# Performance work log

Measured on AMD Instinct MI355X. Metric: run time of the kernel, lower is better.

Reference implementation:

```python
import jax, jax.numpy as jnp
import numpy as np

N_USERS = 100000
N_ITEMS = 100000
N = N_USERS + N_ITEMS
E = 3200000
TXT = 768
GREC = 16
D = 32            # embedding_dim (hardcoded 32 in the torch module)
LAYERS = 3        # len(weight_size)


def setup_inputs() -> dict:
    key = jax.random.key(0)
    ks = jax.random.split(key, 20)
    inp = {}
    inp["edge_row"] = jax.random.randint(ks[0], (E,), 0, N, dtype=jnp.int32)
    inp["edge_col"] = jax.random.randint(ks[1], (E,), 0, N, dtype=jnp.int32)
    # normalized adjacency values (positive, small)
    inp["adj_vals"] = jax.random.uniform(ks[2], (E,), dtype=jnp.float32) * 0.1
    inp["user_name_embs"] = jax.random.normal(ks[3], (N_USERS, TXT), dtype=jnp.float32)
    inp["sent_embs"] = jax.random.normal(ks[4], (N_ITEMS, TXT), dtype=jnp.float32)
    # learned params
    inp["user_emb"] = jax.random.normal(ks[5], (N_USERS, GREC), dtype=jnp.float32) * 0.1
    inp["item_emb"] = jax.random.normal(ks[6], (N_ITEMS, GREC), dtype=jnp.float32) * 0.1
    inp["ue_W1"] = jax.random.normal(ks[7], (TXT, 32), dtype=jnp.float32) * 0.05
    inp["ue_W2"] = jax.random.normal(ks[8], (32, GREC), dtype=jnp.float32) * 0.05
    inp["ie_W1"] = jax.random.normal(ks[9], (TXT, 32), dtype=jnp.float32) * 0.05
    inp["ie_W2"] = jax.random.normal(ks[10], (32, GREC), dtype=jnp.float32) * 0.05
    inp["gc_W"] = jax.random.normal(ks[11], (LAYERS, D, D), dtype=jnp.float32) * 0.1
    inp["gc_b"] = jnp.zeros((LAYERS, D), dtype=jnp.float32)
    inp["bi_W"] = jax.random.normal(ks[12], (LAYERS, D, D), dtype=jnp.float32) * 0.1
    inp["bi_b"] = jnp.zeros((LAYERS, D), dtype=jnp.float32)
    return inp


def _ngcf_forward(edge_row, edge_col, adj_vals, user_name_embs, sent_embs,
                  user_emb, item_emb, ue_W1, ue_W2, ie_W1, ie_W2,
                  gc_W, gc_b, bi_W, bi_b):
    # text encoders (Dropout is identity in eval mode)
    u_created = jax.nn.relu(user_name_embs @ ue_W1) @ ue_W2   # [Nu, 16]
    i_created = jax.nn.relu(sent_embs @ ie_W1) @ ie_W2         # [Ni, 16]
    agg_user = jnp.concatenate([user_emb, u_created], axis=1)  # [Nu, 32]
    agg_item = jnp.concatenate([item_emb, i_created], axis=1)  # [Ni, 32]
    ego = jnp.concatenate([agg_user, agg_item], axis=0)        # [N, 32]

    all_embeddings = [ego]
    for l in range(LAYERS):
        # sparse.mm(adj, ego): gather source rows, scale by edge value, scatter-add
        gathered = adj_vals[:, None] * ego[edge_col]           # [E, 32]
        side = jax.ops.segment_sum(gathered, edge_row, num_segments=N)  # [N, 32]
        sum_emb = jax.nn.leaky_relu(side @ gc_W[l] + gc_b[l])
        bi_emb = jax.nn.leaky_relu((ego * side) @ bi_W[l] + bi_b[l])
        ego = sum_emb + bi_emb                                 # dropout = identity (eval)
        norm = ego / jnp.maximum(
            jnp.linalg.norm(ego, axis=1, keepdims=True), 1e-12)
        all_embeddings.append(norm)
    return jnp.concatenate(all_embeddings, axis=1)             # [N, 32*(LAYERS+1)]


def reference(edge_row, edge_col, adj_vals, user_name_embs, sent_embs,
              user_emb, item_emb, ue_W1, ue_W2, ie_W1, ie_W2,
              gc_W, gc_b, bi_W, bi_b):
    all_e = _ngcf_forward(edge_row, edge_col, adj_vals, user_name_embs, sent_embs,
                          user_emb, item_emb, ue_W1, ue_W2, ie_W1, ie_W2,
                          gc_W, gc_b, bi_W, bi_b)
    u_g = all_e[:N_USERS]
    i_g = all_e[N_USERS:]
    return (u_g, i_g)
```

## Files before the change

kernel.cpp:

```cpp
#include <hip/hip_runtime.h>
#include <cstdint>

#define NU 100000
#define NI 100000
#define NN 200000
#define NE 3200000
#define TXT 768
#define DD 32
#define NRANGE 8
#define ROWS_PER_RANGE (NN / NRANGE)
#define NBJ 313

typedef _Float16 f16x8 __attribute__((ext_vector_type(8)));
typedef _Float16 f16x4 __attribute__((ext_vector_type(4)));
typedef float    f32x4 __attribute__((ext_vector_type(4)));

typedef __attribute__((address_space(1))) const unsigned int guint;
typedef __attribute__((address_space(3))) unsigned int luint;

__device__ __forceinline__ float lrelu(float x) { return x >= 0.f ? x : 0.01f * x; }

__global__ __launch_bounds__(256) void prep_kernel(
    const int* __restrict__ erow,
    const float* __restrict__ uemb, const float* __restrict__ iemb,
    const float* __restrict__ ueW1, const float* __restrict__ ieW1,
    int* __restrict__ cnt,
    _Float16* __restrict__ ego16, float* __restrict__ outp,
    _Float16* __restrict__ w1p)
{
    const int b = blockIdx.x;
    const int tid = threadIdx.x;

    if (b < 2504) {
        const int rlo = (b & 7) * ROWS_PER_RANGE;
        const int rhi = rlo + ROWS_PER_RANGE;
        const int bj  = b >> 3;
        const int4* e4 = (const int4*)erow;
        for (int c = bj * 256 + tid; c < NE / 4; c += NBJ * 256) {
            int4 v = e4[c];
            if (v.x >= rlo && v.x < rhi) atomicAdd(&cnt[v.x], 1);
            if (v.y >= rlo && v.y < rhi) atomicAdd(&cnt[v.y], 1);
            if (v.z >= rlo && v.z < rhi) atomicAdd(&cnt[v.z], 1);
            if (v.w >= rlo && v.w < rhi) atomicAdd(&cnt[v.w], 1);
        }
    } else if (b < 2504 + 3125) {
        int idx = (b - 2504) * 256 + tid;
        if (idx >= NN * 4) return;
        int n = idx >> 2, q = idx & 3;
        float4 v;
        if (n < NU) v = ((const float4*)uemb)[(size_t)n * 4 + q];
        else        v = ((const float4*)iemb)[(size_t)(n - NU) * 4 + q];
        f16x4 h;
        h[0] = (_Float16)v.x; h[1] = (_Float16)v.y;
        h[2] = (_Float16)v.z; h[3] = (_Float16)v.w;
        *(f16x4*)(ego16 + (size_t)n * 32 + q * 4) = h;
        ((float4*)outp)[(size_t)n * 32 + q] = v;
    } else {
        int i = (b - 5629) * 256 + tid;
        int side = (i >= 24576);
        int ii = i - side * 24576;
        const float* W1 = side ? ieW1 : ueW1;
        int j   = ii & 7;
        int ln  = (ii >> 3) & 63;
        int kbH = ii >> 9;
        int kb  = kbH >> 1, H = kbH & 1;
        int k   = kb * 32 + (ln >> 4) * 8 + j;
        int c   = H * 16 + (ln & 15);
        w1p[i] = (_Float16)W1[k * 32 + c];
    }
}

__global__ __launch_bounds__(512, 4) void mlp_mfma_v3(
    const float* __restrict__ Xu, const float* __restrict__ Xi,
    const _Float16* __restrict__ w1pack,
    const float* __restrict__ ueW2, const float* __restrict__ ieW2,
    _Float16* __restrict__ ego16,
    float* __restrict__ outp)
{
    __shared__ float sbuf[16384];

    const int tid  = threadIdx.x;
    const int lane = tid & 63;
    const int wv   = tid >> 6;

    const bool isU = blockIdx.x < 512;
    const float* X  = isU ? Xu : Xi;
    const _Float16* w1p = w1pack + (isU ? 0 : 24576);
    const float* W2 = isU ? ueW2 : ieW2;
    const int node_base = isU ? 0 : NU;
    const int bj = isU ? blockIdx.x : blockIdx.x - 512;

    const int r16 = lane & 15;
    const int cg  = lane >> 4;
    const int rx  = r16 & 7;

    f16x8 bw2;
    #pragma unroll
    for (int j = 0; j < 8; ++j)
        bw2[j] = (_Float16)W2[((lane >> 4) * 8 + j) * 16 + (lane & 15)];

    float* wbuf = &sbuf[wv * 2048];

#define STAGE(bufidx, cc) do {                                                   \
        _Pragma("unroll")                                                        \
        for (int i_ = 0; i_ < 4; ++i_) {                                         \
            int r_ = i_ * 4 + (lane >> 4);                                       \
            int s_ = (lane & 15) ^ (r_ & 7);                                     \
            const float* g_ = xtile + (size_t)r_ * TXT + (cc) * 64 + s_ * 4;     \
            __builtin_amdgcn_global_load_lds((guint*)g_,                         \
                (luint*)(wbuf + (bufidx) * 1024 + i_ * 256), 16, 0, 0);          \
        }                                                                        \
    } while (0)

    const int gw = bj * 8 + wv;
    const int t0 = (int)(((long)gw * 6250) >> 12);
    const int t1 = (int)(((long)(gw + 1) * 6250) >> 12);

    for (int tile = t0; tile < t1; ++tile) {
        const float* xtile = X + (size_t)tile * 16 * TXT;
        asm volatile("s_waitcnt lgkmcnt(0)" ::: "memory");
        STAGE(0, 0);
        STAGE(1, 1);

        f32x4 c0 = {0.f, 0.f, 0.f, 0.f};
        f32x4 c1 = {0.f, 0.f, 0.f, 0.f};

        #pragma unroll
        for (int c = 0; c < 12; ++c) {
            if (c == 11) asm volatile("s_waitcnt vmcnt(0)" ::: "memory");
            else         asm volatile("s_waitcnt vmcnt(4)" ::: "memory");

            #pragma unroll
            for (int k2 = 0; k2 < 2; ++k2) {
                const int kb = c * 2 + k2;
                f16x8 b0 = *(const f16x8*)&w1p[(kb * 2 + 0) * 512 + lane * 8];
                f16x8 b1 = *(const f16x8*)&w1p[(kb * 2 + 1) * 512 + lane * 8];
                const int s0 = k2 * 8 + cg * 2;
                const float* p0 = wbuf + (c & 1) * 1024 + (r16 * 16 + (s0 ^ rx)) * 4;
                const float* p1 = wbuf + (c & 1) * 1024 + (r16 * 16 + ((s0 + 1) ^ rx)) * 4;
                f32x4 xa = *(const f32x4*)p0;
                f32x4 xb = *(const f32x4*)p1;
                f16x8 a;
                a[0] = (_Float16)xa[0]; a[1] = (_Float16)xa[1];
                a[2] = (_Float16)xa[2]; a[3] = (_Float16)xa[3];
                a[4] = (_Float16)xb[0]; a[5] = (_Float16)xb[1];
                a[6] = (_Float16)xb[2]; a[7] = (_Float16)xb[3];
                c0 = __builtin_amdgcn_mfma_f32_16x16x32_f16(a, b0, c0, 0, 0, 0);
                c1 = __builtin_amdgcn_mfma_f32_16x16x32_f16(a, b1, c1, 0, 0, 0);
            }
            if (c < 10) {
                asm volatile("s_waitcnt lgkmcnt(0)" ::: "memory");
                STAGE(c & 1, c + 2);
            }
        }

        _Float16* hb = (_Float16*)wbuf;
        #pragma unroll
        for (int j = 0; j < 4; ++j) {
            int r = (lane >> 4) * 4 + j;
            hb[r * 40 + (lane & 15)]      = (_Float16)fmaxf(c0[j], 0.f);
            hb[r * 40 + (lane & 15) + 16] = (_Float16)fmaxf(c1[j], 0.f);
        }
        const _Float16* ap = &hb[(lane & 15) * 40 + (lane >> 4) * 8];
        f16x4 lo = *(const f16x4*)ap;
        f16x4 hi = *(const f16x4*)(ap + 4);
        f16x8 a2;
        a2[0] = lo[0]; a2[1] = lo[1]; a2[2] = lo[2]; a2[3] = lo[3];
        a2[4] = hi[0]; a2[5] = hi[1]; a2[6] = hi[2]; a2[7] = hi[3];

        f32x4 c2 = {0.f, 0.f, 0.f, 0.f};
        c2 = __builtin_amdgcn_mfma_f32_16x16x32_f16(a2, bw2, c2, 0, 0, 0);

        const int rbase = node_base + tile * 16 + (lane >> 4) * 4;
        const int j2 = lane & 15;
        #pragma unroll
        for (int j = 0; j < 4; ++j) {
            float v = c2[j];
            ego16[(size_t)(rbase + j) * 32  + 16 + j2] = (_Float16)v;
            outp [(size_t)(rbase + j) * 128 + 16 + j2] = v;
        }
    }
#undef STAGE
}

__global__ __launch_bounds__(256) void scan_blk_kernel(const int* __restrict__ cnt,
                                                       int* __restrict__ rp,
                                                       int* __restrict__ bsum)
{
    __shared__ int ts[256];
    const int tid = threadIdx.x;
    const int base = blockIdx.x * 1024 + tid * 4;
    int v0 = (base + 0 < NN) ? cnt[base + 0] : 0;
    int v1 = (base + 1 < NN) ? cnt[base + 1] : 0;
    int v2 = (base + 2 < NN) ? cnt[base + 2] : 0;
    int v3 = (base + 3 < NN) ? cnt[base + 3] : 0;
    int s = v0 + v1 + v2 + v3;
    ts[tid] = s;
    __syncthreads();
    for (int off = 1; off < 256; off <<= 1) {
        int t = (tid >= off) ? ts[tid - off] : 0;
        __syncthreads();
        ts[tid] += t;
        __syncthreads();
    }
    int excl = ts[tid] - s;
    if (base + 0 < NN) rp[base + 0] = excl;
    if (base + 1 < NN) rp[base + 1] = excl + v0;
    if (base + 2 < NN) rp[base + 2] = excl + v0 + v1;
    if (base + 3 < NN) rp[base + 3] = excl + v0 + v1 + v2;
    if (tid == 255) bsum[blockIdx.x] = ts[255];
}

__global__ __launch_bounds__(256) void scan_bsum_kernel(int* __restrict__ bsum, int nblk)
{
    __shared__ int ts[256];
    const int tid = threadIdx.x;
    int v = (tid < nblk) ? bsum[tid] : 0;
    ts[tid] = v;
    __syncthreads();
    for (int off = 1; off < 256; off <<= 1) {
        int t = (tid >= off) ? ts[tid - off] : 0;
        __syncthreads();
        ts[tid] += t;
        __syncthreads();
    }
    if (tid < nblk) bsum[tid] = ts[tid] - v;
}

__global__ __launch_bounds__(256) void add_off_kernel(int* __restrict__ rp,
                                                      const int* __restrict__ bsum,
                                                      int* __restrict__ cur)
{
    int i = blockIdx.x * 256 + threadIdx.x;
    if (i < NN) {
        int v = rp[i] + bsum[i >> 10];
        rp[i] = v;
        cur[i] = v;
    }
    if (i == 0) rp[NN] = NE;
}

__global__ __launch_bounds__(256) void fill_ranged_kernel(const int* __restrict__ erow,
                                                          const int* __restrict__ ecol,
                                                          const float* __restrict__ eval,
                                                          int* __restrict__ cur,
                                                          uint2* __restrict__ recs)
{
    const int rlo = (blockIdx.x & 7) * ROWS_PER_RANGE;
    const int rhi = rlo + ROWS_PER_RANGE;
    const int bj  = blockIdx.x >> 3;
    const int4* e4 = (const int4*)erow;
    for (int c = bj * 256 + threadIdx.x; c < NE / 4; c += NBJ * 256) {
        int4 v = e4[c];
        int base = c * 4;
        if (v.x >= rlo && v.x < rhi) {
            int pos = atomicAdd(&cur[v.x], 1);
            recs[pos] = make_uint2((unsigned)ecol[base+0] | ((unsigned)(v.x & 63) << 18),
                                   __float_as_uint(eval[base+0]));
        }
        if (v.y >= rlo && v.y < rhi) {
            int pos = atomicAdd(&cur[v.y], 1);
            recs[pos] = make_uint2((unsigned)ecol[base+1] | ((unsigned)(v.y & 63) << 18),
                                   __float_as_uint(eval[base+1]));
        }
        if (v.z >= rlo && v.z < rhi) {
            int pos = atomicAdd(&cur[v.z], 1);
            recs[pos] = make_uint2((unsigned)ecol[base+2] | ((unsigned)(v.z & 63) << 18),
                                   __float_as_uint(eval[base+2]));
        }
        if (v.w >= rlo && v.w < rhi) {
            int pos = atomicAdd(&cur[v.w], 1);
            recs[pos] = make_uint2((unsigned)ecol[base+3] | ((unsigned)(v.w & 63) << 18),
                                   __float_as_uint(eval[base+3]));
        }
    }
}

__global__ __launch_bounds__(256) void pull_update_v2(
    const int* __restrict__ rp, const uint2* __restrict__ recs,
    const _Float16* __restrict__ egoIn, _Float16* __restrict__ egoOut,
    float* __restrict__ outp,
    const float* __restrict__ gcW, const float* __restrict__ gcb,
    const float* __restrict__ biW, const float* __restrict__ bib, int l)
{
    __shared__ float acc[64][33];
    __shared__ float Wg[32][36];
    __shared__ float Wb[32][36];
    __shared__ float bgs[32], bbs[32];

    const int tid = threadIdx.x;
    for (int i = tid; i < 64 * 33; i += 256) ((float*)acc)[i] = 0.f;
    for (int i = tid; i < 1024; i += 256) {
        Wg[i >> 5][i & 31] = gcW[l * 1024 + i];
        Wb[i >> 5][i & 31] = biW[l * 1024 + i];
    }
    if (tid < 32) { bgs[tid] = gcb[l * 32 + tid]; bbs[tid] = bib[l * 32 + tid]; }

    const int r0 = blockIdx.x * 64;
    const int eBeg = rp[r0], eEnd = rp[r0 + 64];
    __syncthreads();

    const int cnt = eEnd - eBeg;
    const int s   = tid >> 3;
    const int q   = tid & 7;
    const int L   = (cnt + 31) >> 5;
    const int e0  = eBeg + s * L;
    const int e1  = min(e0 + L, eEnd);

    float4 a4 = make_float4(0.f, 0.f, 0.f, 0.f);
    int curRl = -1;

    auto PROC = [&](uint2 rr, f16x4 vv) {
        int rl = rr.x >> 18;
        float a = __uint_as_float(rr.y);
        if (rl != curRl) {
            if (curRl >= 0) {
                atomicAdd(&acc[curRl][q * 4 + 0], a4.x);
                atomicAdd(&acc[curRl][q * 4 + 1], a4.y);
                atomicAdd(&acc[curRl][q * 4 + 2], a4.z);
                atomicAdd(&acc[curRl][q * 4 + 3], a4.w);
            }
            a4 = make_float4(0.f, 0.f, 0.f, 0.f);
            curRl = rl;
        }
        a4.x += a * (float)vv[0];
        a4.y += a * (float)vv[1];
        a4.z += a * (float)vv[2];
        a4.w += a * (float)vv[3];
    };

    int e = e0;
    for (; e + 4 <= e1; e += 4) {
        uint2 r0r = recs[e],     r1r = recs[e + 1];
        uint2 r2r = recs[e + 2], r3r = recs[e + 3];
        f16x4 v0 = *(const f16x4*)(egoIn + (size_t)(r0r.x & 0x3FFFF) * 32 + q * 4);
        f16x4 v1 = *(const f16x4*)(egoIn + (size_t)(r1r.x & 0x3FFFF) * 32 + q * 4);
        f16x4 v2 = *(const f16x4*)(egoIn + (size_t)(r2r.x & 0x3FFFF) * 32 + q * 4);
        f16x4 v3 = *(const f16x4*)(egoIn + (size_t)(r3r.x & 0x3FFFF) * 32 + q * 4);
        PROC(r0r, v0); PROC(r1r, v1); PROC(r2r, v2); PROC(r3r, v3);
    }
    for (; e < e1; ++e) {
        uint2 rr = recs[e];
        f16x4 vv = *(const f16x4*)(egoIn + (size_t)(rr.x & 0x3FFFF) * 32 + q * 4);
        PROC(rr, vv);
    }
    if (curRl >= 0) {
        atomicAdd(&acc[curRl][q * 4 + 0], a4.x);
        atomicAdd(&acc[curRl][q * 4 + 1], a4.y);
        atomicAdd(&acc[curRl][q * 4 + 2], a4.z);
        atomicAdd(&acc[curRl][q * 4 + 3], a4.w);
    }
    __syncthreads();

    const int r    = tid >> 2;
    const int c    = tid & 3;
    const int node = r0 + r;
    const int j0   = c * 8;

    const _Float16* er = egoIn + (size_t)node * 32;
    f16x8 ev0 = *(const f16x8*)er;
    f16x8 ev1 = *(const f16x8*)(er + 8);
    f16x8 ev2 = *(const f16x8*)(er + 16);
    f16x8 ev3 = *(const f16x8*)(er + 24);

    float A[8], B[8];
    #pragma unroll
    for (int jj = 0; jj < 8; ++jj) { A[jj] = bgs[j0 + jj]; B[jj] = bbs[j0 + jj]; }

    #pragma unroll
    for (int kq = 0; kq < 4; ++kq) {
        #pragma unroll
        for (int kk = 0; kk < 8; ++kk) {
            const int k = kq * 8 + kk;
            float sk = acc[r][k];
            float evk = (kq == 0) ? (float)ev0[kk] : (kq == 1) ? (float)ev1[kk]
                      : (kq == 2) ? (float)ev2[kk] : (float)ev3[kk];
            float ek = sk * evk;
            f32x4 g0 = *(const f32x4*)&Wg[k][j0];
            f32x4 g1 = *(const f32x4*)&Wg[k][j0 + 4];
            f32x4 b0 = *(const f32x4*)&Wb[k][j0];
            f32x4 b1 = *(const f32x4*)&Wb[k][j0 + 4];
            A[0] += sk * g0[0]; A[1] += sk * g0[1]; A[2] += sk * g0[2]; A[3] += sk * g0[3];
            A[4] += sk * g1[0]; A[5] += sk * g1[1]; A[6] += sk * g1[2]; A[7] += sk * g1[3];
            B[0] += ek * b0[0]; B[1] += ek * b0[1]; B[2] += ek * b0[2]; B[3] += ek * b0[3];
            B[4] += ek * b1[0]; B[5] += ek * b1[1]; B[6] += ek * b1[2]; B[7] += ek * b1[3];
        }
    }

    float v[8];
    float ss = 0.f;
    #pragma unroll
    for (int jj = 0; jj < 8; ++jj) {
        float x = lrelu(A[jj]) + lrelu(B[jj]);
        v[jj] = x;
        ss += x * x;
    }
    ss += __shfl_xor(ss, 1, 64);
    ss += __shfl_xor(ss, 2, 64);
    float inv = 1.0f / fmaxf(sqrtf(ss), 1e-12f);

    f16x8 h;
    #pragma unroll
    for (int jj = 0; jj < 8; ++jj) h[jj] = (_Float16)v[jj];
    *(f16x8*)(egoOut + (size_t)node * 32 + j0) = h;

    float* op = outp + (size_t)node * 128 + (size_t)(l + 1) * 32 + j0;
    float4 o0 = make_float4(v[0] * inv, v[1] * inv, v[2] * inv, v[3] * inv);
    float4 o1 = make_float4(v[4] * inv, v[5] * inv, v[6] * inv, v[7] * inv);
    *(float4*)op       = o0;
    *(float4*)(op + 4) = o1;
}

extern "C" void kernel_launch(void* const* d_in, const int* in_sizes, int n_in,
                              void* d_out, int out_size, void* d_ws, size_t ws_size,
                              hipStream_t stream)
{
    const int*   erow = (const int*)d_in[0];
    const int*   ecol = (const int*)d_in[1];
    const float* evalp = (const float*)d_in[2];
    const float* une  = (const float*)d_in[3];
    const float* se   = (const float*)d_in[4];
    const float* uemb = (const float*)d_in[5];
    const float* iemb = (const float*)d_in[6];
    const float* ueW1 = (const float*)d_in[7];
    const float* ueW2 = (const float*)d_in[8];
    const float* ieW1 = (const float*)d_in[9];
    const float* ieW2 = (const float*)d_in[10];
    const float* gcW  = (const float*)d_in[11];
    const float* gcb  = (const float*)d_in[12];
    const float* biW  = (const float*)d_in[13];
    const float* bib  = (const float*)d_in[14];
    float* outp = (float*)d_out;

    _Float16* egoA16 = (_Float16*)d_ws;
    _Float16* egoB16 = egoA16 + (size_t)NN * 32;
    uint2* recs = (uint2*)(egoB16 + (size_t)NN * 32);
    int*   cnt  = (int*)(recs + (size_t)NE);
    int*   rp   = cnt + NN;
    int*   cur  = rp + NN + 1;
    int*   bsum = cur + NN;
    _Float16* w1pack = (_Float16*)(bsum + 256);

    const size_t need = (size_t)((char*)(w1pack + 49152) - (char*)d_ws);
    if (ws_size < need) return;

    hipMemsetAsync(cnt, 0, (size_t)NN * sizeof(int), stream);
    prep_kernel<<<5821, 256, 0, stream>>>(erow, uemb, iemb, ueW1, ieW1,
                                          cnt, egoA16, outp, w1pack);

    mlp_mfma_v3<<<1024, 512, 0, stream>>>(une, se, w1pack, ueW2, ieW2,
                                          egoA16, outp);

    const int NBLK = (NN + 1023) / 1024;
    scan_blk_kernel<<<NBLK, 256, 0, stream>>>(cnt, rp, bsum);
    scan_bsum_kernel<<<1, 256, 0, stream>>>(bsum, NBLK);
    add_off_kernel<<<(NN + 255) / 256, 256, 0, stream>>>(rp, bsum, cur);
    fill_ranged_kernel<<<NRANGE * NBJ, 256, 0, stream>>>(erow, ecol, evalp, cur, recs);

    const _Float16* egoIn = egoA16;
    _Float16* egoOut = egoB16;
    for (int l = 0; l < 3; ++l) {
        pull_update_v2<<<NN / 64, 256, 0, stream>>>(rp, recs, egoIn, egoOut, outp,
                                                    gcW, gcb, biW, bib, l);
        const _Float16* t = egoOut; egoOut = (_Float16*)egoIn; egoIn = t;
    }
}
```

Measured before the change: 739.2 us.

## Split MLP K across waves with cross-wave reduction, vectorize fill, deepen gather unroll

```diff
diff --git a/kernel.cpp b/kernel.cpp
--- a/kernel.cpp
+++ b/kernel.cpp
@@ -6,7 +6,6 @@
 #define NN 200000
 #define NE 3200000
 #define TXT 768
-#define DD 32
 #define NRANGE 8
 #define ROWS_PER_RANGE (NN / NRANGE)
 #define NBJ 313
@@ -19,6 +18,11 @@
 typedef __attribute__((address_space(3))) unsigned int luint;
 
 __device__ __forceinline__ float lrelu(float x) { return x >= 0.f ? x : 0.01f * x; }
+
+#define MEMFENCE asm volatile("" ::: "memory")
+#define WAIT_VM(N)  asm volatile("s_waitcnt vmcnt(" #N ")" ::: "memory")
+#define WAIT_LGKM0  asm volatile("s_waitcnt lgkmcnt(0)" ::: "memory")
+#define BARRIER     do { __builtin_amdgcn_s_barrier(); MEMFENCE; } while (0)
 
 __global__ __launch_bounds__(256) void prep_kernel(
     const int* __restrict__ erow,
@@ -70,117 +74,133 @@
     }
 }
 
-__global__ __launch_bounds__(512, 4) void mlp_mfma_v3(
+__global__ __launch_bounds__(256, 4) void mlp_mfma_v4(
     const float* __restrict__ Xu, const float* __restrict__ Xi,
     const _Float16* __restrict__ w1pack,
     const float* __restrict__ ueW2, const float* __restrict__ ieW2,
     _Float16* __restrict__ ego16,
     float* __restrict__ outp)
 {
-    __shared__ float sbuf[16384];
-
-    const int tid  = threadIdx.x;
-    const int lane = tid & 63;
-    const int wv   = tid >> 6;
-
-    const bool isU = blockIdx.x < 512;
-    const float* X  = isU ? Xu : Xi;
-    const _Float16* w1p = w1pack + (isU ? 0 : 24576);
-    const float* W2 = isU ? ueW2 : ieW2;
-    const int node_base = isU ? 0 : NU;
-    const int bj = isU ? blockIdx.x : blockIdx.x - 512;
-
-    const int r16 = lane & 15;
-    const int cg  = lane >> 4;
-    const int rx  = r16 & 7;
-
-    f16x8 bw2;
+    __shared__ float buf[2][4096];
+    __shared__ float part[3][512];
+    __shared__ _Float16 hbuf[640];
+
+    const int tid   = threadIdx.x;
+    const int lane  = tid & 63;
+    const int wv    = tid >> 6;
+    const int row16 = lane & 15;
+    const int cg    = lane >> 4;
+    const int rx7   = row16 & 7;
+
+    f16x8 bw2u, bw2i;
     #pragma unroll
-    for (int j = 0; j < 8; ++j)
-        bw2[j] = (_Float16)W2[((lane >> 4) * 8 + j) * 16 + (lane & 15)];
-
-    float* wbuf = &sbuf[wv * 2048];
-
-#define STAGE(bufidx, cc) do {                                                   \
-        _Pragma("unroll")                                                        \
-        for (int i_ = 0; i_ < 4; ++i_) {                                         \
-            int r_ = i_ * 4 + (lane >> 4);                                       \
-            int s_ = (lane & 15) ^ (r_ & 7);                                     \
-            const float* g_ = xtile + (size_t)r_ * TXT + (cc) * 64 + s_ * 4;     \
-            __builtin_amdgcn_global_load_lds((guint*)g_,                         \
-                (luint*)(wbuf + (bufidx) * 1024 + i_ * 256), 16, 0, 0);          \
-        }                                                                        \
-    } while (0)
-
-    const int gw = bj * 8 + wv;
-    const int t0 = (int)(((long)gw * 6250) >> 12);
-    const int t1 = (int)(((long)(gw + 1) * 6250) >> 12);
-
-    for (int tile = t0; tile < t1; ++tile) {
-        const float* xtile = X + (size_t)tile * 16 * TXT;
-        asm volatile("s_waitcnt lgkmcnt(0)" ::: "memory");
+    for (int j = 0; j < 8; ++j) {
+        bw2u[j] = (_Float16)ueW2[((lane >> 4) * 8 + j) * 16 + (lane & 15)];
+        bw2i[j] = (_Float16)ieW2[((lane >> 4) * 8 + j) * 16 + (lane & 15)];
+    }
+
+    const int tA = (int)(((long)blockIdx.x * 12500) >> 10);
+    const int tB = (int)(((long)(blockIdx.x + 1) * 12500) >> 10);
+
+    for (int t = tA; t < tB; ++t) {
+        const bool isU = t < 6250;
+        const int tile = isU ? t : t - 6250;
+        const float* xt = (isU ? Xu : Xi) + (size_t)tile * 16 * TXT;
+        const _Float16* w1p = w1pack + (isU ? 0 : 24576);
+
+#define STAGE(bb, cc) do {                                                      \
+            _Pragma("unroll")                                                   \
+            for (int i_ = 0; i_ < 4; ++i_) {                                    \
+                const int r_ = wv * 4 + i_;                                     \
+                const float* g_ = xt + (size_t)r_ * TXT + (cc) * 256            \
+                                  + ((lane ^ (r_ & 7)) << 2);                   \
+                __builtin_amdgcn_global_load_lds((guint*)g_,                    \
+                    (luint*)&buf[bb][r_ * 256], 16, 0, 0);                      \
+            }                                                                   \
+        } while (0)
+
+#define MCHUNK(bb, cc) do {                                                     \
+            _Pragma("unroll")                                                   \
+            for (int kl2 = 0; kl2 < 2; ++kl2) {                                 \
+                const int kbl = wv * 2 + kl2;                                   \
+                const int kb  = (cc) * 8 + kbl;                                 \
+                f16x8 b0 = *(const f16x8*)&w1p[(kb * 2 + 0) * 512 + lane * 8];  \
+                f16x8 b1 = *(const f16x8*)&w1p[(kb * 2 + 1) * 512 + lane * 8];  \
+                const int u0 = kbl * 8 + cg * 2;                                \
+                f32x4 xa = *(const f32x4*)&buf[bb][row16 * 256 + ((u0 ^ rx7) << 2)]; \
+                f32x4 xb = *(const f32x4*)&buf[bb][row16 * 256 + (((u0 + 1) ^ rx7) << 2)]; \
+                f16x8 a;                                                        \
+                a[0] = (_Float16)xa[0]; a[1] = (_Float16)xa[1];                 \
+                a[2] = (_Float16)xa[2]; a[3] = (_Float16)xa[3];                 \
+                a[4] = (_Float16)xb[0]; a[5] = (_Float16)xb[1];                 \
+                a[6] = (_Float16)xb[2]; a[7] = (_Float16)xb[3];                 \
+                c0 = __builtin_amdgcn_mfma_f32_16x16x32_f16(a, b0, c0, 0, 0, 0); \
+                c1 = __builtin_amdgcn_mfma_f32_16x16x32_f16(a, b1, c1, 0, 0, 0); \
+            }                                                                   \
+        } while (0)
+
+        f32x4 c0 = {0.f, 0.f, 0.f, 0.f};
+        f32x4 c1 = {0.f, 0.f, 0.f, 0.f};
+
         STAGE(0, 0);
         STAGE(1, 1);
-
-        f32x4 c0 = {0.f, 0.f, 0.f, 0.f};
-        f32x4 c1 = {0.f, 0.f, 0.f, 0.f};
-
-        #pragma unroll
-        for (int c = 0; c < 12; ++c) {
-            if (c == 11) asm volatile("s_waitcnt vmcnt(0)" ::: "memory");
-            else         asm volatile("s_waitcnt vmcnt(4)" ::: "memory");
-
+        WAIT_VM(4);
+        BARRIER;
+        MCHUNK(0, 0);
+        WAIT_LGKM0;
+        BARRIER;
+        STAGE(0, 2);
+        WAIT_VM(4);
+        BARRIER;
+        MCHUNK(1, 1);
+        WAIT_LGKM0;
+        WAIT_VM(0);
+        BARRIER;
+        MCHUNK(0, 2);
+        WAIT_LGKM0;
+
+        if (wv > 0) {
+            *(f32x4*)&part[wv - 1][lane * 8]     = c0;
+            *(f32x4*)&part[wv - 1][lane * 8 + 4] = c1;
+            WAIT_LGKM0;
+        }
+        BARRIER;
+
+        if (wv == 0) {
             #pragma unroll
-            for (int k2 = 0; k2 < 2; ++k2) {
-                const int kb = c * 2 + k2;
-                f16x8 b0 = *(const f16x8*)&w1p[(kb * 2 + 0) * 512 + lane * 8];
-                f16x8 b1 = *(const f16x8*)&w1p[(kb * 2 + 1) * 512 + lane * 8];
-                const int s0 = k2 * 8 + cg * 2;
-                const float* p0 = wbuf + (c & 1) * 1024 + (r16 * 16 + (s0 ^ rx)) * 4;
-                const float* p1 = wbuf + (c & 1) * 1024 + (r16 * 16 + ((s0 + 1) ^ rx)) * 4;
-                f32x4 xa = *(const f32x4*)p0;
-                f32x4 xb = *(const f32x4*)p1;
-                f16x8 a;
-                a[0] = (_Float16)xa[0]; a[1] = (_Float16)xa[1];
-                a[2] = (_Float16)xa[2]; a[3] = (_Float16)xa[3];
-                a[4] = (_Float16)xb[0]; a[5] = (_Float16)xb[1];
-                a[6] = (_Float16)xb[2]; a[7] = (_Float16)xb[3];
-                c0 = __builtin_amdgcn_mfma_f32_16x16x32_f16(a, b0, c0, 0, 0, 0);
-                c1 = __builtin_amdgcn_mfma_f32_16x16x32_f16(a, b1, c1, 0, 0, 0);
+            for (int p = 0; p < 3; ++p) {
+                f32x4 pa = *(const f32x4*)&part[p][lane * 8];
+                f32x4 pb = *(const f32x4*)&part[p][lane * 8 + 4];
+                c0 += pa; c1 += pb;
             }
-            if (c < 10) {
-                asm volatile("s_waitcnt lgkmcnt(0)" ::: "memory");
-                STAGE(c & 1, c + 2);
+            #pragma unroll
+            for (int j = 0; j < 4; ++j) {
+                int r = cg * 4 + j;
+                hbuf[r * 40 + row16]      = (_Float16)fmaxf(c0[j], 0.f);
+                hbuf[r * 40 + row16 + 16] = (_Float16)fmaxf(c1[j], 0.f);
             }
-        }
-
-        _Float16* hb = (_Float16*)wbuf;
-        #pragma unroll
-        for (int j = 0; j < 4; ++j) {
-            int r = (lane >> 4) * 4 + j;
-            hb[r * 40 + (lane & 15)]      = (_Float16)fmaxf(c0[j], 0.f);
-            hb[r * 40 + (lane & 15) + 16] = (_Float16)fmaxf(c1[j], 0.f);
-        }
-        const _Float16* ap = &hb[(lane & 15) * 40 + (lane >> 4) * 8];
-        f16x4 lo = *(const f16x4*)ap;
-        f16x4 hi = *(const f16x4*)(ap + 4);
-        f16x8 a2;
-        a2[0] = lo[0]; a2[1] = lo[1]; a2[2] = lo[2]; a2[3] = lo[3];
-        a2[4] = hi[0]; a2[5] = hi[1]; a2[6] = hi[2]; a2[7] = hi[3];
-
-        f32x4 c2 = {0.f, 0.f, 0.f, 0.f};
-        c2 = __builtin_amdgcn_mfma_f32_16x16x32_f16(a2, bw2, c2, 0, 0, 0);
-
-        const int rbase = node_base + tile * 16 + (lane >> 4) * 4;
-        const int j2 = lane & 15;
-        #pragma unroll
-        for (int j = 0; j < 4; ++j) {
-            float v = c2[j];
-            ego16[(size_t)(rbase + j) * 32  + 16 + j2] = (_Float16)v;
-            outp [(size_t)(rbase + j) * 128 + 16 + j2] = v;
-        }
-    }
+            const _Float16* ap = &hbuf[row16 * 40 + cg * 8];
+            f16x4 lo = *(const f16x4*)ap;
+            f16x4 hi = *(const f16x4*)(ap + 4);
+            f16x8 a2;
+            a2[0] = lo[0]; a2[1] = lo[1]; a2[2] = lo[2]; a2[3] = lo[3];
+            a2[4] = hi[0]; a2[5] = hi[1]; a2[6] = hi[2]; a2[7] = hi[3];
+
+            f32x4 c2 = {0.f, 0.f, 0.f, 0.f};
+            f16x8 bw2 = isU ? bw2u : bw2i;
+            c2 = __builtin_amdgcn_mfma_f32_16x16x32_f16(a2, bw2, c2, 0, 0, 0);
+
+            const int rbase = (isU ? 0 : NU) + tile * 16 + cg * 4;
+            #pragma unroll
+            for (int j = 0; j < 4; ++j) {
+                float v = c2[j];
+                ego16[(size_t)(rbase + j) * 32  + 16 + row16] = (_Float16)v;
+                outp [(size_t)(rbase + j) * 128 + 16 + row16] = v;
+            }
+        }
 #undef STAGE
+#undef MCHUNK
+    }
 }
 
 __global__ __launch_bounds__(256) void scan_blk_kernel(const int* __restrict__ cnt,
@@ -249,29 +269,32 @@
     const int rlo = (blockIdx.x & 7) * ROWS_PER_RANGE;
     const int rhi = rlo + ROWS_PER_RANGE;
     const int bj  = blockIdx.x >> 3;
-    const int4* e4 = (const int4*)erow;
+    const int4*   e4 = (const int4*)erow;
+    const int4*   c4 = (const int4*)ecol;
+    const float4* f4 = (const float4*)eval;
     for (int c = bj * 256 + threadIdx.x; c < NE / 4; c += NBJ * 256) {
-        int4 v = e4[c];
-        int base = c * 4;
+        int4 v   = e4[c];
+        int4 cc  = c4[c];
+        float4 vv = f4[c];
         if (v.x >= rlo && v.x < rhi) {
             int pos = atomicAdd(&cur[v.x], 1);
-            recs[pos] = make_uint2((unsigned)ecol[base+0] | ((unsigned)(v.x & 63) << 18),
-                                   __float_as_uint(eval[base+0]));
+            recs[pos] = make_uint2((unsigned)cc.x | ((unsigned)(v.x & 63) << 18),
+                                   __float_as_uint(vv.x));
         }
         if (v.y >= rlo && v.y < rhi) {
             int pos = atomicAdd(&cur[v.y], 1);
-            recs[pos] = make_uint2((unsigned)ecol[base+1] | ((unsigned)(v.y & 63) << 18),
-                                   __float_as_uint(eval[base+1]));
+            recs[pos] = make_uint2((unsigned)cc.y | ((unsigned)(v.y & 63) << 18),
+                                   __float_as_uint(vv.y));
         }
         if (v.z >= rlo && v.z < rhi) {
             int pos = atomicAdd(&cur[v.z], 1);
-            recs[pos] = make_uint2((unsigned)ecol[base+2] | ((unsigned)(v.z & 63) << 18),
-                                   __float_as_uint(eval[base+2]));
+            recs[pos] = make_uint2((unsigned)cc.z | ((unsigned)(v.z & 63) << 18),
+                                   __float_as_uint(vv.z));
         }
         if (v.w >= rlo && v.w < rhi) {
             int pos = atomicAdd(&cur[v.w], 1);
-            recs[pos] = make_uint2((unsigned)ecol[base+3] | ((unsigned)(v.w & 63) << 18),
-                                   __float_as_uint(eval[base+3]));
+            recs[pos] = make_uint2((unsigned)cc.w | ((unsigned)(v.w & 63) << 18),
+                                   __float_as_uint(vv.w));
         }
     }
 }
@@ -330,14 +353,21 @@
     };
 
     int e = e0;
-    for (; e + 4 <= e1; e += 4) {
+    for (; e + 8 <= e1; e += 8) {
         uint2 r0r = recs[e],     r1r = recs[e + 1];
         uint2 r2r = recs[e + 2], r3r = recs[e + 3];
+        uint2 r4r = recs[e + 4], r5r = recs[e + 5];
+        uint2 r6r = recs[e + 6], r7r = recs[e + 7];
         f16x4 v0 = *(const f16x4*)(egoIn + (size_t)(r0r.x & 0x3FFFF) * 32 + q * 4);
         f16x4 v1 = *(const f16x4*)(egoIn + (size_t)(r1r.x & 0x3FFFF) * 32 + q * 4);
         f16x4 v2 = *(const f16x4*)(egoIn + (size_t)(r2r.x & 0x3FFFF) * 32 + q * 4);
         f16x4 v3 = *(const f16x4*)(egoIn + (size_t)(r3r.x & 0x3FFFF) * 32 + q * 4);
+        f16x4 v4 = *(const f16x4*)(egoIn + (size_t)(r4r.x & 0x3FFFF) * 32 + q * 4);
+        f16x4 v5 = *(const f16x4*)(egoIn + (size_t)(r5r.x & 0x3FFFF) * 32 + q * 4);
+        f16x4 v6 = *(const f16x4*)(egoIn + (size_t)(r6r.x & 0x3FFFF) * 32 + q * 4);
+        f16x4 v7 = *(const f16x4*)(egoIn + (size_t)(r7r.x & 0x3FFFF) * 32 + q * 4);
         PROC(r0r, v0); PROC(r1r, v1); PROC(r2r, v2); PROC(r3r, v3);
+        PROC(r4r, v4); PROC(r5r, v5); PROC(r6r, v6); PROC(r7r, v7);
     }
     for (; e < e1; ++e) {
         uint2 rr = recs[e];
@@ -448,7 +478,7 @@
     prep_kernel<<<5821, 256, 0, stream>>>(erow, uemb, iemb, ueW1, ieW1,
                                           cnt, egoA16, outp, w1pack);
 
-    mlp_mfma_v3<<<1024, 512, 0, stream>>>(une, se, w1pack, ueW2, ieW2,
+    mlp_mfma_v4<<<1024, 256, 0, stream>>>(une, se, w1pack, ueW2, ieW2,
                                           egoA16, outp);
 
     const int NBLK = (NN + 1023) / 1024;
```

Measured after the change: 698.2 us. 1.06x faster.
